# Kernel optimization log

Hardware: AMD Instinct MI355X
Metric: run time of the kernel (lower is better)

## Reference

```python
import jax, jax.numpy as jnp
import numpy as np

D_IN, D_OUT, SEQ, BATCH = 768, 768, 4096, 4

def setup_inputs() -> dict:
    key = jax.random.key(0)
    k0, k1, k2, k3 = jax.random.split(key, 4)
    s = 1.0 / np.sqrt(D_IN)
    return {
        "input_batch": jax.random.normal(k0, (BATCH, SEQ, D_IN), dtype=jnp.float32),
        "Wq": jax.random.uniform(k1, (D_OUT, D_IN), jnp.float32, -s, s),
        "Wk": jax.random.uniform(k2, (D_OUT, D_IN), jnp.float32, -s, s),
        "Wv": jax.random.uniform(k3, (D_OUT, D_IN), jnp.float32, -s, s),
    }

def reference(input_batch, Wq, Wk, Wv):
    B, N, d_in = input_batch.shape
    q = jnp.einsum('bnd,od->bno', input_batch, Wq)  # [B,N,d_out]
    k = jnp.einsum('bnd,od->bno', input_batch, Wk)
    v = jnp.einsum('bnd,od->bno', input_batch, Wv)
    scores = jnp.einsum('bqo,bko->bqk', q, k)  # [B,N,N]
    causal = jnp.tril(jnp.ones((N, N), dtype=bool))
    scores = jnp.where(causal, scores, -jnp.inf)
    # note: original scales by d_in (input embedding dim), not d_out
    weights = jax.nn.softmax(scores / jnp.sqrt(jnp.asarray(d_in, scores.dtype)), axis=-1)
    return jnp.einsum('bqk,bko->bqo', weights, v)
```

## Files before the change

### kernel.cpp

```cpp
#include <hip/hip_runtime.h>
#include <hip/hip_bf16.h>
#include <stdint.h>

#define NSEQ 4096
#define DDIM 768
#define NB   4
#define NTRI 528
#define BLKE 16384

typedef short short8 __attribute__((ext_vector_type(8)));
typedef float f32x16 __attribute__((ext_vector_type(16)));

__device__ __forceinline__ unsigned short f2bf(float f) {
    unsigned int u = __float_as_uint(f);
    u += 0x7fffu + ((u >> 16) & 1u);
    return (unsigned short)(u >> 16);
}
__device__ __forceinline__ short8 cvt8(const float* __restrict__ p) {
    float4 x = *(const float4*)p;
    float4 y = *(const float4*)(p + 4);
    union { short8 s; __hip_bfloat162 h[4]; } u;
    u.h[0] = __float22bfloat162_rn(make_float2(x.x, x.y));
    u.h[1] = __float22bfloat162_rn(make_float2(x.z, x.w));
    u.h[2] = __float22bfloat162_rn(make_float2(y.x, y.y));
    u.h[3] = __float22bfloat162_rn(make_float2(y.z, y.w));
    return u.s;
}

typedef const __attribute__((address_space(1))) unsigned int ga_u32;
typedef __attribute__((address_space(3))) unsigned int ls_u32;
__device__ __forceinline__ void gload_lds16(const void* g, void* l) {
    __builtin_amdgcn_global_load_lds((ga_u32*)(uintptr_t)g, (ls_u32*)(uintptr_t)l, 16, 0, 0);
}

__device__ __forceinline__ void stage_tile(const unsigned short* gbase, int stride,
                                           unsigned short* lds, int tid) {
    const int lane = tid & 63, wv = tid >> 6;
    const int r8  = lane >> 3;
    const int cl  = (lane & 7) * 8;
#pragma unroll
    for (int t = 0; t < 4; ++t) {
        const int row = wv * 32 + t * 8 + r8;
        const int csw = (((lane & 7) ^ r8 ^ t) & 7) * 8;
        gload_lds16(gbase + (size_t)row * stride + csw, lds + row * 64 + cl);
    }
}

__device__ __forceinline__ void mma_tiles(const unsigned short* As, const unsigned short* Bs,
                                          f32x16 acc[2][2], int wm, int wn, int lane) {
    const int r32 = lane & 31;
    const int hi  = lane >> 5;
    const int sw  = (lane & 7) ^ ((lane >> 3) & 3);
#pragma unroll
    for (int c = 0; c < 4; ++c) {
        const int chunk = (((c * 2 + hi) ^ sw) & 7) * 8;
        short8 af[2], bg[2];
#pragma unroll
        for (int mt = 0; mt < 2; ++mt)
            af[mt] = *(const short8*)(As + (wm * 64 + mt * 32 + r32) * 64 + chunk);
#pragma unroll
        for (int nt = 0; nt < 2; ++nt)
            bg[nt] = *(const short8*)(Bs + (wn * 64 + nt * 32 + r32) * 64 + chunk);
#pragma unroll
        for (int mt = 0; mt < 2; ++mt)
#pragma unroll
            for (int nt = 0; nt < 2; ++nt)
                acc[mt][nt] = __builtin_amdgcn_mfma_f32_32x32x16_bf16(af[mt], bg[nt], acc[mt][nt], 0, 0, 0);
    }
}

__device__ __forceinline__ int crow(int reg, int hi) {
    return (reg & 3) + 8 * (reg >> 2) + 4 * hi;
}

__global__ __launch_bounds__(256)
void convert_kernel(const float* __restrict__ X, const float* __restrict__ Wq,
                    const float* __restrict__ Wk, const float* __restrict__ Wv,
                    unsigned short* __restrict__ Xb, unsigned short* __restrict__ Wb,
                    float* __restrict__ L, unsigned int* __restrict__ counter)
{
    const int bid = blockIdx.x;
    if (bid == 0 && threadIdx.x == 0) *counter = 0u;
    if (bid >= 7008) {
        const int idx = (bid - 7008) * 1024 + threadIdx.x * 4;
        *(float4*)(L + idx) = make_float4(0.f, 0.f, 0.f, 0.f);
        return;
    }
    const float* src; unsigned short* dst; size_t off;
    if (bid < 6144) { src = X; dst = Xb; off = (size_t)bid * 2048; }
    else {
        const int wbid = bid - 6144;
        const int wi = wbid / 288;
        src = (wi == 0) ? Wq : ((wi == 1) ? Wk : Wv);
        dst = Wb + (size_t)wi * (DDIM * DDIM);
        off = (size_t)(wbid - wi * 288) * 2048;
    }
    const size_t i = off + (size_t)threadIdx.x * 8;
    *(short8*)(dst + i) = cvt8(src + i);
}

__global__ __launch_bounds__(256)
void qkv_gemm(const unsigned short* __restrict__ Xb, const unsigned short* __restrict__ Wb,
              unsigned short* __restrict__ Qb, unsigned short* __restrict__ Kb,
              unsigned short* __restrict__ Vtb)
{
    const int tid = threadIdx.x, lane = tid & 63, wv = tid >> 6;
    const int r32 = lane & 31, hi = lane >> 5, wm = wv >> 1, wn = wv & 1;
    const int bx = (blockIdx.x & 7) * 16 + (blockIdx.x >> 3);
    const int m0 = bx * 128, n0 = blockIdx.y * 128, widx = blockIdx.z;
    const unsigned short* A = Xb + (size_t)m0 * DDIM;
    const unsigned short* B = Wb + (size_t)widx * (DDIM * DDIM) + (size_t)n0 * DDIM;

    __shared__ __align__(16) unsigned short As[128 * 64];
    __shared__ __align__(16) unsigned short Bs[128 * 64];

    f32x16 acc[2][2] = {};

    for (int kt = 0; kt < 12; ++kt) {
        stage_tile(A + kt * 64, DDIM, As, tid);
        stage_tile(B + kt * 64, DDIM, Bs, tid);
        __syncthreads();
        mma_tiles(As, Bs, acc, wm, wn, lane);
        __syncthreads();
    }

    const int m_base = m0 + wm * 64, o_base = n0 + wn * 64;
    if (widx < 2) {
        unsigned short* dst = (widx == 0) ? Qb : Kb;
#pragma unroll
        for (int mt = 0; mt < 2; ++mt)
#pragma unroll
            for (int nt = 0; nt < 2; ++nt)
#pragma unroll
                for (int reg = 0; reg < 16; ++reg)
                    dst[(size_t)(m_base + mt * 32 + crow(reg, hi)) * DDIM +
                        (o_base + nt * 32 + r32)] = f2bf(acc[mt][nt][reg]);
    } else {
        const int bb = m0 >> 12;
        const int n_seq0 = (m0 & (NSEQ - 1)) + wm * 64;
#pragma unroll
        for (int mt = 0; mt < 2; ++mt)
#pragma unroll
            for (int nt = 0; nt < 2; ++nt) {
                const int o = o_base + nt * 32 + r32;
#pragma unroll
                for (int b4 = 0; b4 < 4; ++b4) {
                    ushort4 pk;
                    pk.x = f2bf(acc[mt][nt][b4 * 4 + 0]);
                    pk.y = f2bf(acc[mt][nt][b4 * 4 + 1]);
                    pk.z = f2bf(acc[mt][nt][b4 * 4 + 2]);
                    pk.w = f2bf(acc[mt][nt][b4 * 4 + 3]);
                    const int n = n_seq0 + mt * 32 + b4 * 8 + hi * 4;
                    *(ushort4*)(Vtb + ((size_t)(bb * DDIM + o)) * NSEQ + n) = pk;
                }
            }
    }
}

__global__ __launch_bounds__(256)
void gemm_s(const unsigned short* __restrict__ Qb, const unsigned short* __restrict__ Kb,
            unsigned short* __restrict__ Sbuf, float* __restrict__ L)
{
    const float c2 = 0.05205877475f;
    const int tid = threadIdx.x, lane = tid & 63, wv = tid >> 6;
    const int r32 = lane & 31, hi = lane >> 5, wm = wv >> 1, wn = wv & 1;
    const int idx = (blockIdx.x & 7) * 66 + (blockIdx.x >> 3);
    const int bb = blockIdx.y;
    int qb = (int)((sqrtf(8.f * idx + 1.f) - 1.f) * 0.5f);
    while ((qb + 1) * (qb + 2) / 2 <= idx) ++qb;
    while (qb * (qb + 1) / 2 > idx) --qb;
    const int kb = idx - qb * (qb + 1) / 2;

    const unsigned short* A = Qb + ((size_t)bb * NSEQ + qb * 128) * DDIM;
    const unsigned short* B = Kb + ((size_t)bb * NSEQ + kb * 128) * DDIM;

    __shared__ __align__(16) unsigned short As[128 * 64];
    __shared__ __align__(16) unsigned short Bs[128 * 64];

    f32x16 acc[2][2] = {};

    for (int kt = 0; kt < 12; ++kt) {
        stage_tile(A + kt * 64, DDIM, As, tid);
        stage_tile(B + kt * 64, DDIM, Bs, tid);
        __syncthreads();
        mma_tiles(As, Bs, acc, wm, wn, lane);
        __syncthreads();
    }

    unsigned short* Sblk = Sbuf + ((size_t)(bb * NTRI + idx)) * BLKE;
    float* Lrow = L + (size_t)bb * NSEQ + qb * 128;
    const bool diag = (qb == kb);
#pragma unroll
    for (int mt = 0; mt < 2; ++mt)
#pragma unroll
        for (int rp = 0; rp < 8; ++rp) {
            const int reg0 = rp * 2, reg1 = rp * 2 + 1;
            const int row0 = wm * 64 + mt * 32 + crow(reg0, hi);
            const int row1 = row0 + 1;
            float vs0 = 0.f, vs1 = 0.f;
#pragma unroll
            for (int nt = 0; nt < 2; ++nt) {
                const int col = wn * 64 + nt * 32 + r32;
                float e0 = (diag && col > row0) ? 0.f : exp2f(acc[mt][nt][reg0] * c2);
                float e1 = (diag && col > row1) ? 0.f : exp2f(acc[mt][nt][reg1] * c2);
                union { __hip_bfloat162 h; ushort2 u; } cv;
                cv.h = __float22bfloat162_rn(make_float2(e0, e1));
                Sblk[row0 * 128 + col] = cv.u.x;
                Sblk[row1 * 128 + col] = cv.u.y;
                vs0 += e0;
                vs1 += e1;
            }
#pragma unroll
            for (int s = 1; s < 32; s <<= 1) {
                vs0 += __shfl_xor(vs0, s);
                vs1 += __shfl_xor(vs1, s);
            }
            if (r32 == 0) {
                atomicAdd(&Lrow[row0], vs0);
                atomicAdd(&Lrow[row1], vs1);
            }
        }
}

__global__ __launch_bounds__(256)
void gemm_pv(const unsigned short* __restrict__ P, const unsigned short* __restrict__ Vt,
             const float* __restrict__ L, float* __restrict__ Out,
             unsigned int* __restrict__ counter)
{
    const int tid = threadIdx.x, lane = tid & 63, wv = tid >> 6;
    const int r32 = lane & 31, hi = lane >> 5, wm = wv >> 1, wn = wv & 1;

    __shared__ __align__(16) unsigned short As[128 * 64];
    __shared__ __align__(16) unsigned short Bs[128 * 64];
    __shared__ float Linv[128];
    __shared__ unsigned int item_s;

    for (;;) {
        if (tid == 0) item_s = atomicAdd(counter, 1u);
        __syncthreads();
        const unsigned int item = item_s;
        if (item >= 768u) return;

        const int t = (int)(item / 24u);
        const int qb = 31 - t;
        const int rem = (int)(item - (unsigned)t * 24u);
        const int bb = rem / 6, ob = rem % 6;
        const size_t triq = (size_t)qb * (qb + 1) / 2;
        const unsigned short* Pbat = P + (size_t)bb * NTRI * BLKE;
        const unsigned short* Bbase = Vt + ((size_t)(bb * DDIM + ob * 128)) * NSEQ;
        const int niter = (qb + 1) * 2;

        if (tid < 128) Linv[tid] = 1.0f / L[(size_t)bb * NSEQ + qb * 128 + tid];

        f32x16 acc[2][2] = {};

        for (int it = 0; it < niter; ++it) {
            const int k0 = it * 64;
            const int kblk = k0 >> 7, cb = k0 & 64;
            stage_tile(Pbat + (triq + kblk) * BLKE + cb, 128, As, tid);
            stage_tile(Bbase + k0, NSEQ, Bs, tid);
            __syncthreads();
            mma_tiles(As, Bs, acc, wm, wn, lane);
            __syncthreads();
        }

        const int o_base = ob * 128 + wn * 64;
#pragma unroll
        for (int mt = 0; mt < 2; ++mt)
#pragma unroll
            for (int nt = 0; nt < 2; ++nt)
#pragma unroll
                for (int reg = 0; reg < 16; ++reg) {
                    const int rl = wm * 64 + mt * 32 + crow(reg, hi);
                    const int q = qb * 128 + rl;
                    Out[((size_t)(bb * NSEQ + q)) * DDIM + (o_base + nt * 32 + r32)] =
                        acc[mt][nt][reg] * Linv[rl];
                }
    }
}

extern "C" void kernel_launch(void* const* d_in, const int* in_sizes, int n_in,
                              void* d_out, int out_size, void* d_ws, size_t ws_size,
                              hipStream_t stream)
{
    const float* X  = (const float*)d_in[0];
    const float* Wq = (const float*)d_in[1];
    const float* Wk = (const float*)d_in[2];
    const float* Wv = (const float*)d_in[3];
    float* Out = (float*)d_out;

    const size_t E = (size_t)NB * NSEQ * DDIM;
    char* ws = (char*)d_ws;
    unsigned short* Qb  = (unsigned short*)ws;
    unsigned short* Kb  = Qb + E;
    unsigned short* Vtb = Kb + E;
    unsigned short* Sbuf = Vtb + E;
    unsigned short* Xb  = Sbuf;
    unsigned short* Wb  = Xb + E;
    float* L = (float*)(ws + 3 * E * 2 + (size_t)NB * NTRI * BLKE * 2);
    unsigned int* counter = (unsigned int*)(L + (size_t)NB * NSEQ);

    convert_kernel<<<7024, 256, 0, stream>>>(X, Wq, Wk, Wv, Xb, Wb, L, counter);
    qkv_gemm<<<dim3(128, 6, 3), 256, 0, stream>>>(Xb, Wb, Qb, Kb, Vtb);
    gemm_s<<<dim3(528, NB), 256, 0, stream>>>(Qb, Kb, Sbuf, L);
    gemm_pv<<<512, 256, 0, stream>>>(Sbuf, Vtb, L, Out, counter);
}
```

Baseline: 369.4 us.

## Compute softmax row sums in PV via ones-MFMA, drop atomics and block swizzle

Removes the per-row exp-sum shuffles and global atomicAdds from the score kernel and the L buffer zeroing, and instead accumulates row sums inside the PV kernel by multiplying each P fragment against a bf16 ones vector with an extra MFMA. Normalization then uses a hardware reciprocal of that accumulator. It also drops the blockIdx swizzling in the QKV and score GEMMs. This trades atomic traffic and an extra buffer for 50% more MFMA work in the PV loop, and may lose L2 locality from the removed swizzle.

```diff
diff --git a/kernel.cpp b/kernel.cpp
--- a/kernel.cpp
+++ b/kernel.cpp
@@ -69,6 +69,32 @@
     }
 }
 
+__device__ __forceinline__ void mma_tiles_pv(const unsigned short* As, const unsigned short* Bs,
+                                             f32x16 acc[2][2], f32x16 accS[2], short8 ones,
+                                             int wm, int wn, int lane) {
+    const int r32 = lane & 31;
+    const int hi  = lane >> 5;
+    const int sw  = (lane & 7) ^ ((lane >> 3) & 3);
+#pragma unroll
+    for (int c = 0; c < 4; ++c) {
+        const int chunk = (((c * 2 + hi) ^ sw) & 7) * 8;
+        short8 af[2], bg[2];
+#pragma unroll
+        for (int mt = 0; mt < 2; ++mt)
+            af[mt] = *(const short8*)(As + (wm * 64 + mt * 32 + r32) * 64 + chunk);
+#pragma unroll
+        for (int nt = 0; nt < 2; ++nt)
+            bg[nt] = *(const short8*)(Bs + (wn * 64 + nt * 32 + r32) * 64 + chunk);
+#pragma unroll
+        for (int mt = 0; mt < 2; ++mt) {
+#pragma unroll
+            for (int nt = 0; nt < 2; ++nt)
+                acc[mt][nt] = __builtin_amdgcn_mfma_f32_32x32x16_bf16(af[mt], bg[nt], acc[mt][nt], 0, 0, 0);
+            accS[mt] = __builtin_amdgcn_mfma_f32_32x32x16_bf16(af[mt], ones, accS[mt], 0, 0, 0);
+        }
+    }
+}
+
 __device__ __forceinline__ int crow(int reg, int hi) {
     return (reg & 3) + 8 * (reg >> 2) + 4 * hi;
 }
@@ -77,15 +103,10 @@
 void convert_kernel(const float* __restrict__ X, const float* __restrict__ Wq,
                     const float* __restrict__ Wk, const float* __restrict__ Wv,
                     unsigned short* __restrict__ Xb, unsigned short* __restrict__ Wb,
-                    float* __restrict__ L, unsigned int* __restrict__ counter)
+                    unsigned int* __restrict__ counter)
 {
     const int bid = blockIdx.x;
     if (bid == 0 && threadIdx.x == 0) *counter = 0u;
-    if (bid >= 7008) {
-        const int idx = (bid - 7008) * 1024 + threadIdx.x * 4;
-        *(float4*)(L + idx) = make_float4(0.f, 0.f, 0.f, 0.f);
-        return;
-    }
     const float* src; unsigned short* dst; size_t off;
     if (bid < 6144) { src = X; dst = Xb; off = (size_t)bid * 2048; }
     else {
@@ -106,8 +127,7 @@
 {
     const int tid = threadIdx.x, lane = tid & 63, wv = tid >> 6;
     const int r32 = lane & 31, hi = lane >> 5, wm = wv >> 1, wn = wv & 1;
-    const int bx = (blockIdx.x & 7) * 16 + (blockIdx.x >> 3);
-    const int m0 = bx * 128, n0 = blockIdx.y * 128, widx = blockIdx.z;
+    const int m0 = blockIdx.x * 128, n0 = blockIdx.y * 128, widx = blockIdx.z;
     const unsigned short* A = Xb + (size_t)m0 * DDIM;
     const unsigned short* B = Wb + (size_t)widx * (DDIM * DDIM) + (size_t)n0 * DDIM;
 
@@ -159,13 +179,12 @@
 
 __global__ __launch_bounds__(256)
 void gemm_s(const unsigned short* __restrict__ Qb, const unsigned short* __restrict__ Kb,
-            unsigned short* __restrict__ Sbuf, float* __restrict__ L)
+            unsigned short* __restrict__ Sbuf)
 {
     const float c2 = 0.05205877475f;
     const int tid = threadIdx.x, lane = tid & 63, wv = tid >> 6;
     const int r32 = lane & 31, hi = lane >> 5, wm = wv >> 1, wn = wv & 1;
-    const int idx = (blockIdx.x & 7) * 66 + (blockIdx.x >> 3);
-    const int bb = blockIdx.y;
+    const int idx = blockIdx.x, bb = blockIdx.y;
     int qb = (int)((sqrtf(8.f * idx + 1.f) - 1.f) * 0.5f);
     while ((qb + 1) * (qb + 2) / 2 <= idx) ++qb;
     while (qb * (qb + 1) / 2 > idx) --qb;
@@ -188,7 +207,6 @@
     }
 
     unsigned short* Sblk = Sbuf + ((size_t)(bb * NTRI + idx)) * BLKE;
-    float* Lrow = L + (size_t)bb * NSEQ + qb * 128;
     const bool diag = (qb == kb);
 #pragma unroll
     for (int mt = 0; mt < 2; ++mt)
@@ -197,7 +215,6 @@
             const int reg0 = rp * 2, reg1 = rp * 2 + 1;
             const int row0 = wm * 64 + mt * 32 + crow(reg0, hi);
             const int row1 = row0 + 1;
-            float vs0 = 0.f, vs1 = 0.f;
 #pragma unroll
             for (int nt = 0; nt < 2; ++nt) {
                 const int col = wn * 64 + nt * 32 + r32;
@@ -207,32 +224,23 @@
                 cv.h = __float22bfloat162_rn(make_float2(e0, e1));
                 Sblk[row0 * 128 + col] = cv.u.x;
                 Sblk[row1 * 128 + col] = cv.u.y;
-                vs0 += e0;
-                vs1 += e1;
-            }
-#pragma unroll
-            for (int s = 1; s < 32; s <<= 1) {
-                vs0 += __shfl_xor(vs0, s);
-                vs1 += __shfl_xor(vs1, s);
-            }
-            if (r32 == 0) {
-                atomicAdd(&Lrow[row0], vs0);
-                atomicAdd(&Lrow[row1], vs1);
             }
         }
 }
 
 __global__ __launch_bounds__(256)
 void gemm_pv(const unsigned short* __restrict__ P, const unsigned short* __restrict__ Vt,
-             const float* __restrict__ L, float* __restrict__ Out,
-             unsigned int* __restrict__ counter)
+             float* __restrict__ Out, unsigned int* __restrict__ counter)
 {
     const int tid = threadIdx.x, lane = tid & 63, wv = tid >> 6;
     const int r32 = lane & 31, hi = lane >> 5, wm = wv >> 1, wn = wv & 1;
 
+    short8 ones;
+#pragma unroll
+    for (int j = 0; j < 8; ++j) ones[j] = (short)0x3F80;
+
     __shared__ __align__(16) unsigned short As[128 * 64];
     __shared__ __align__(16) unsigned short Bs[128 * 64];
-    __shared__ float Linv[128];
     __shared__ unsigned int item_s;
 
     for (;;) {
@@ -250,9 +258,8 @@
         const unsigned short* Bbase = Vt + ((size_t)(bb * DDIM + ob * 128)) * NSEQ;
         const int niter = (qb + 1) * 2;
 
-        if (tid < 128) Linv[tid] = 1.0f / L[(size_t)bb * NSEQ + qb * 128 + tid];
-
         f32x16 acc[2][2] = {};
+        f32x16 accS[2] = {};
 
         for (int it = 0; it < niter; ++it) {
             const int k0 = it * 64;
@@ -260,7 +267,7 @@
             stage_tile(Pbat + (triq + kblk) * BLKE + cb, 128, As, tid);
             stage_tile(Bbase + k0, NSEQ, Bs, tid);
             __syncthreads();
-            mma_tiles(As, Bs, acc, wm, wn, lane);
+            mma_tiles_pv(As, Bs, acc, accS, ones, wm, wn, lane);
             __syncthreads();
         }
 
@@ -268,14 +275,15 @@
 #pragma unroll
         for (int mt = 0; mt < 2; ++mt)
 #pragma unroll
-            for (int nt = 0; nt < 2; ++nt)
-#pragma unroll
-                for (int reg = 0; reg < 16; ++reg) {
-                    const int rl = wm * 64 + mt * 32 + crow(reg, hi);
-                    const int q = qb * 128 + rl;
+            for (int reg = 0; reg < 16; ++reg) {
+                const int rl = wm * 64 + mt * 32 + crow(reg, hi);
+                const int q = qb * 128 + rl;
+                const float rs = __builtin_amdgcn_rcpf(accS[mt][reg]);
+#pragma unroll
+                for (int nt = 0; nt < 2; ++nt)
                     Out[((size_t)(bb * NSEQ + q)) * DDIM + (o_base + nt * 32 + r32)] =
-                        acc[mt][nt][reg] * Linv[rl];
-                }
+                        acc[mt][nt][reg] * rs;
+            }
     }
 }
 
@@ -297,11 +305,10 @@
     unsigned short* Sbuf = Vtb + E;
     unsigned short* Xb  = Sbuf;
     unsigned short* Wb  = Xb + E;
-    float* L = (float*)(ws + 3 * E * 2 + (size_t)NB * NTRI * BLKE * 2);
-    unsigned int* counter = (unsigned int*)(L + (size_t)NB * NSEQ);
-
-    convert_kernel<<<7024, 256, 0, stream>>>(X, Wq, Wk, Wv, Xb, Wb, L, counter);
+    unsigned int* counter = (unsigned int*)(ws + 3 * E * 2 + (size_t)NB * NTRI * BLKE * 2);
+
+    convert_kernel<<<7008, 256, 0, stream>>>(X, Wq, Wk, Wv, Xb, Wb, counter);
     qkv_gemm<<<dim3(128, 6, 3), 256, 0, stream>>>(Xb, Wb, Qb, Kb, Vtb);
-    gemm_s<<<dim3(528, NB), 256, 0, stream>>>(Qb, Kb, Sbuf, L);
-    gemm_pv<<<512, 256, 0, stream>>>(Sbuf, Vtb, L, Out, counter);
-}
+    gemm_s<<<dim3(528, NB), 256, 0, stream>>>(Qb, Kb, Sbuf);
+    gemm_pv<<<512, 256, 0, stream>>>(Sbuf, Vtb, Out, counter);
+}
```

After: 362.2 us. 1.02x faster.

## Split row-sum into separate kernel, drop block swizzles, raise PV occupancy

Applied to the files above, without the earlier changes.

Moves the softmax denominator accumulation out of the score GEMM epilogue into a new kernel that rereads the bf16 score blocks and sums rows, removing shuffle reductions and atomics from gemm_s. It also removes the XCD-style block index swizzles from the QKV and score GEMMs, sets launch bounds of 3 blocks per SM on the PV kernel, and launches twice as many persistent PV blocks. The new pass rereads the whole score buffer, adding memory traffic and a launch. The denominator is now summed from rounded bf16 values rather than fp32, which slightly changes numerics.

```diff
diff --git a/kernel.cpp b/kernel.cpp
--- a/kernel.cpp
+++ b/kernel.cpp
@@ -15,6 +15,9 @@
     unsigned int u = __float_as_uint(f);
     u += 0x7fffu + ((u >> 16) & 1u);
     return (unsigned short)(u >> 16);
+}
+__device__ __forceinline__ float bf2f(unsigned short h) {
+    return __uint_as_float(((unsigned int)h) << 16);
 }
 __device__ __forceinline__ short8 cvt8(const float* __restrict__ p) {
     float4 x = *(const float4*)p;
@@ -106,8 +109,7 @@
 {
     const int tid = threadIdx.x, lane = tid & 63, wv = tid >> 6;
     const int r32 = lane & 31, hi = lane >> 5, wm = wv >> 1, wn = wv & 1;
-    const int bx = (blockIdx.x & 7) * 16 + (blockIdx.x >> 3);
-    const int m0 = bx * 128, n0 = blockIdx.y * 128, widx = blockIdx.z;
+    const int m0 = blockIdx.x * 128, n0 = blockIdx.y * 128, widx = blockIdx.z;
     const unsigned short* A = Xb + (size_t)m0 * DDIM;
     const unsigned short* B = Wb + (size_t)widx * (DDIM * DDIM) + (size_t)n0 * DDIM;
 
@@ -159,13 +161,12 @@
 
 __global__ __launch_bounds__(256)
 void gemm_s(const unsigned short* __restrict__ Qb, const unsigned short* __restrict__ Kb,
-            unsigned short* __restrict__ Sbuf, float* __restrict__ L)
+            unsigned short* __restrict__ Sbuf)
 {
     const float c2 = 0.05205877475f;
     const int tid = threadIdx.x, lane = tid & 63, wv = tid >> 6;
     const int r32 = lane & 31, hi = lane >> 5, wm = wv >> 1, wn = wv & 1;
-    const int idx = (blockIdx.x & 7) * 66 + (blockIdx.x >> 3);
-    const int bb = blockIdx.y;
+    const int idx = blockIdx.x, bb = blockIdx.y;
     int qb = (int)((sqrtf(8.f * idx + 1.f) - 1.f) * 0.5f);
     while ((qb + 1) * (qb + 2) / 2 <= idx) ++qb;
     while (qb * (qb + 1) / 2 > idx) --qb;
@@ -188,7 +189,6 @@
     }
 
     unsigned short* Sblk = Sbuf + ((size_t)(bb * NTRI + idx)) * BLKE;
-    float* Lrow = L + (size_t)bb * NSEQ + qb * 128;
     const bool diag = (qb == kb);
 #pragma unroll
     for (int mt = 0; mt < 2; ++mt)
@@ -197,7 +197,6 @@
             const int reg0 = rp * 2, reg1 = rp * 2 + 1;
             const int row0 = wm * 64 + mt * 32 + crow(reg0, hi);
             const int row1 = row0 + 1;
-            float vs0 = 0.f, vs1 = 0.f;
 #pragma unroll
             for (int nt = 0; nt < 2; ++nt) {
                 const int col = wn * 64 + nt * 32 + r32;
@@ -207,22 +206,35 @@
                 cv.h = __float22bfloat162_rn(make_float2(e0, e1));
                 Sblk[row0 * 128 + col] = cv.u.x;
                 Sblk[row1 * 128 + col] = cv.u.y;
-                vs0 += e0;
-                vs1 += e1;
-            }
-#pragma unroll
-            for (int s = 1; s < 32; s <<= 1) {
-                vs0 += __shfl_xor(vs0, s);
-                vs1 += __shfl_xor(vs1, s);
-            }
-            if (r32 == 0) {
-                atomicAdd(&Lrow[row0], vs0);
-                atomicAdd(&Lrow[row1], vs1);
             }
         }
 }
 
 __global__ __launch_bounds__(256)
+void gemm_l(const unsigned short* __restrict__ Sbuf, float* __restrict__ L)
+{
+    const int tid = threadIdx.x;
+    const int idx = blockIdx.x, bb = blockIdx.y;
+    int qb = (int)((sqrtf(8.f * idx + 1.f) - 1.f) * 0.5f);
+    while ((qb + 1) * (qb + 2) / 2 <= idx) ++qb;
+    while (qb * (qb + 1) / 2 > idx) --qb;
+
+    const unsigned short* Sblk = Sbuf + ((size_t)(bb * NTRI + idx)) * BLKE;
+    const unsigned short* rowp = Sblk + (tid >> 1) * 128 + (tid & 1) * 64;
+
+    float s = 0.f;
+#pragma unroll
+    for (int j = 0; j < 8; ++j) {
+        short8 v = *(const short8*)(rowp + j * 8);
+#pragma unroll
+        for (int e = 0; e < 8; ++e) s += bf2f((unsigned short)v[e]);
+    }
+    s += __shfl_xor(s, 1);
+    if ((tid & 1) == 0)
+        atomicAdd(&L[(size_t)bb * NSEQ + qb * 128 + (tid >> 1)], s);
+}
+
+__global__ __launch_bounds__(256, 3)
 void gemm_pv(const unsigned short* __restrict__ P, const unsigned short* __restrict__ Vt,
              const float* __restrict__ L, float* __restrict__ Out,
              unsigned int* __restrict__ counter)
@@ -302,6 +314,7 @@
 
     convert_kernel<<<7024, 256, 0, stream>>>(X, Wq, Wk, Wv, Xb, Wb, L, counter);
     qkv_gemm<<<dim3(128, 6, 3), 256, 0, stream>>>(Xb, Wb, Qb, Kb, Vtb);
-    gemm_s<<<dim3(528, NB), 256, 0, stream>>>(Qb, Kb, Sbuf, L);
-    gemm_pv<<<512, 256, 0, stream>>>(Sbuf, Vtb, L, Out, counter);
-}
+    gemm_s<<<dim3(528, NB), 256, 0, stream>>>(Qb, Kb, Sbuf);
+    gemm_l<<<dim3(528, NB), 256, 0, stream>>>(Sbuf, L);
+    gemm_pv<<<1024, 256, 0, stream>>>(Sbuf, Vtb, L, Out, counter);
+}
```

Measured after the change: 413.2 us. 1.12x slower.
